# Optimization experiments

Hardware: AMD Instinct MI355X
Metric: run time of the kernel (lower is better)

## Reference

```python
import jax, jax.numpy as jnp
import numpy as np
import math

D_MODEL = 1024
NUM_HEADS = 16
HEAD_DIM = D_MODEL // NUM_HEADS  # 64
THETA = 10000.0
BATCH = 2
SEQ = 2048


def setup_inputs() -> dict:
    key = jax.random.key(0)
    ks = jax.random.split(key, 5)
    scale = 0.02
    return {
        "in_features": jax.random.normal(ks[0], (BATCH, SEQ, D_MODEL), jnp.float32),
        "q_proj": jax.random.normal(ks[1], (D_MODEL, D_MODEL), jnp.float32) * scale,
        "k_proj": jax.random.normal(ks[2], (D_MODEL, D_MODEL), jnp.float32) * scale,
        "v_proj": jax.random.normal(ks[3], (D_MODEL, D_MODEL), jnp.float32) * scale,
        "o_proj": jax.random.normal(ks[4], (D_MODEL, D_MODEL), jnp.float32) * scale,
        "token_positions": jnp.arange(SEQ, dtype=jnp.int32),
    }


def _rope(x, token_positions):
    # x: [b, h, s, head_dim]; interleaved even/odd rotation
    half = HEAD_DIM // 2
    inv_freq = 1.0 / (THETA ** (2.0 * jnp.arange(half, dtype=x.dtype) / HEAD_DIM))
    angle = token_positions.astype(x.dtype)[:, None] * inv_freq[None, :]  # [s, half]
    cos, sin = jnp.cos(angle), jnp.sin(angle)
    x_e, x_o = x[..., ::2], x[..., 1::2]
    r_e = x_e * cos - x_o * sin
    r_o = x_e * sin + x_o * cos
    # interleave back: [..., s, half, 2] -> [..., s, head_dim]
    return jnp.stack([r_e, r_o], axis=-1).reshape(x.shape)


def reference(in_features, q_proj, k_proj, v_proj, o_proj, token_positions):
    b, s, _ = in_features.shape
    # projections: weight layout is [d_out, d_in]
    Q = jnp.einsum('bsd,kd->bsk', in_features, q_proj)
    K = jnp.einsum('bsd,kd->bsk', in_features, k_proj)
    V = jnp.einsum('bsd,kd->bsk', in_features, v_proj)
    # split heads: [b, h, s, head_dim]
    Q = Q.reshape(b, s, NUM_HEADS, HEAD_DIM).transpose(0, 2, 1, 3)
    K = K.reshape(b, s, NUM_HEADS, HEAD_DIM).transpose(0, 2, 1, 3)
    V = V.reshape(b, s, NUM_HEADS, HEAD_DIM).transpose(0, 2, 1, 3)
    Q = _rope(Q, token_positions)
    K = _rope(K, token_positions)
    scores = jnp.einsum('bhnd,bhmd->bhnm', Q, K) / math.sqrt(HEAD_DIM)
    causal = jnp.tril(jnp.ones((s, s), dtype=bool))  # [s, s]
    scores = jnp.where(causal[None, None], scores, -jnp.inf)
    attn = jax.nn.softmax(scores, axis=-1)
    out = jnp.einsum('bhnm,bhmd->bhnd', attn, V)
    out = out.transpose(0, 2, 1, 3).reshape(b, s, D_MODEL)
    return jnp.einsum('bsv,dv->bsd', out, o_proj)
```

## Files before the change

kernel.cpp:

```cpp
#include <hip/hip_runtime.h>
#include <hip/hip_bf16.h>

#define D_MODEL 1024
#define NHEAD   16
#define HDIM    64
#define SEQQ    2048
#define NBATCH  2
#define MROWS   (NBATCH * SEQQ)

typedef unsigned short u16;
typedef __attribute__((ext_vector_type(8))) short short8;
typedef __attribute__((ext_vector_type(4))) float floatx4;

__device__ __forceinline__ u16 f2b(float f) {
    union { __hip_bfloat16 h; u16 u; } cv;
    cv.h = __float2bfloat16(f);
    return cv.u;
}
__device__ __forceinline__ float b2f(u16 u) {
    return __uint_as_float(((unsigned int)u) << 16);
}
__device__ __forceinline__ short8 load8(const u16* p) {
    return *reinterpret_cast<const short8*>(p);
}
__device__ __forceinline__ void async_cp16(const void* g, void* l) {
    __builtin_amdgcn_global_load_lds(
        (const __attribute__((address_space(1))) void*)g,
        (__attribute__((address_space(3))) void*)l, 16, 0, 0);
}

__global__ void cvt_all(const float* __restrict__ X,
                        const float* __restrict__ w0, const float* __restrict__ w1,
                        const float* __restrict__ w2, const float* __restrict__ w3,
                        u16* __restrict__ xo,
                        u16* __restrict__ o0, u16* __restrict__ o1,
                        u16* __restrict__ o2, u16* __restrict__ o3) {
    const int z = blockIdx.y;
    const int n4 = (D_MODEL * D_MODEL) / 4;
    const float* in;
    u16* out;
    if (z < 4) { in = X + (size_t)z * n4 * 4;  out = xo + (size_t)z * n4 * 4; }
    else {
        in  = (z == 4) ? w0 : (z == 5) ? w1 : (z == 6) ? w2 : w3;
        out = (z == 4) ? o0 : (z == 5) ? o1 : (z == 6) ? o2 : o3;
    }
    const int i = blockIdx.x * 256 + threadIdx.x;
    float4 v = reinterpret_cast<const float4*>(in)[i];
    ushort4 o;
    o.x = f2b(v.x); o.y = f2b(v.y); o.z = f2b(v.z); o.w = f2b(v.w);
    reinterpret_cast<ushort4*>(out)[i] = o;
}

__global__ __launch_bounds__(256) void gemm_qkv(
    const u16* __restrict__ A,
    const u16* __restrict__ B0, const u16* __restrict__ B1, const u16* __restrict__ B2,
    u16* __restrict__ C0, u16* __restrict__ C1, u16* __restrict__ C2)
{
    const int K = D_MODEL, N = D_MODEL;
    const u16* Bt = (blockIdx.z == 0) ? B0 : (blockIdx.z == 1 ? B1 : B2);
    u16*       Cp = (blockIdx.z == 0) ? C0 : (blockIdx.z == 1 ? C1 : C2);

    __shared__ __attribute__((aligned(16))) u16 As[128 * 32];
    __shared__ __attribute__((aligned(16))) u16 Bs[128 * 32];

    const int tid  = threadIdx.x;
    const int w    = tid >> 6;
    const int lane = tid & 63;
    const int l15  = lane & 15;
    const int quad = lane >> 4;
    const int wm   = w >> 1, wn = w & 1;
    const int tm   = blockIdx.x * 128, tn = blockIdx.y * 128;

    floatx4 acc[4][4];
#pragma unroll
    for (int i = 0; i < 4; i++)
#pragma unroll
        for (int j = 0; j < 4; j++) {
            floatx4 z = {0.f, 0.f, 0.f, 0.f};
            acc[i][j] = z;
        }

    const int srow = lane >> 2;
    const int scol = (lane & 3) * 8;

    for (int k0 = 0; k0 < K; k0 += 32) {
#pragma unroll
        for (int ch = w; ch < 8; ch += 4) {
            async_cp16(A  + (size_t)(tm + ch * 16 + srow) * K + k0 + scol, &As[ch * 512]);
            async_cp16(Bt + (size_t)(tn + ch * 16 + srow) * K + k0 + scol, &Bs[ch * 512]);
        }
        __syncthreads();

        short8 af[4], bfr[4];
#pragma unroll
        for (int mi = 0; mi < 4; mi++)
            af[mi] = load8(&As[(wm * 64 + mi * 16 + l15) * 32 + quad * 8]);
#pragma unroll
        for (int ni = 0; ni < 4; ni++)
            bfr[ni] = load8(&Bs[(wn * 64 + ni * 16 + l15) * 32 + quad * 8]);
#pragma unroll
        for (int mi = 0; mi < 4; mi++)
#pragma unroll
            for (int ni = 0; ni < 4; ni++)
                acc[mi][ni] = __builtin_amdgcn_mfma_f32_16x16x32_bf16(af[mi], bfr[ni], acc[mi][ni], 0, 0, 0);
        __syncthreads();
    }

#pragma unroll
    for (int mi = 0; mi < 4; mi++)
#pragma unroll
        for (int ni = 0; ni < 4; ni++)
#pragma unroll
            for (int rg = 0; rg < 4; rg++) {
                int row = tm + wm * 64 + mi * 16 + quad * 4 + rg;
                int col = tn + wn * 64 + ni * 16 + l15;
                Cp[(size_t)row * N + col] = f2b(acc[mi][ni][rg]);
            }
}

__global__ void rope_qk(const u16* __restrict__ Qraw, const u16* __restrict__ Kraw,
                        const int* __restrict__ pos, u16* __restrict__ Qt, u16* __restrict__ Kt)
{
    const int gid = blockIdx.x * 256 + threadIdx.x;
    const int j = gid & 31;
    const int s = (gid >> 5) & (SEQQ - 1);
    const int h = (gid >> 16) & (NHEAD - 1);
    const int b = gid >> 20;

    const float p   = (float)pos[s];
    const float inv = expf(-(float)j * (9.210340371976184f / 32.0f));
    float sn, cs;
    sincosf(p * inv, &sn, &cs);

    const size_t ioff = ((size_t)(b * SEQQ + s)) * D_MODEL + h * HDIM + 2 * j;
    const ushort2 qp = *reinterpret_cast<const ushort2*>(&Qraw[ioff]);
    const ushort2 kp = *reinterpret_cast<const ushort2*>(&Kraw[ioff]);
    const float qe = b2f(qp.x), qo = b2f(qp.y);
    const float ke = b2f(kp.x), ko = b2f(kp.y);

    const size_t ooff = (((size_t)(b * NHEAD + h)) * SEQQ + s) * HDIM + 2 * j;
    ushort2 qr;
    qr.x = f2b((qe * cs - qo * sn) * 0.125f);
    qr.y = f2b((qe * sn + qo * cs) * 0.125f);
    ushort2 kr;
    kr.x = f2b(ke * cs - ko * sn);
    kr.y = f2b(ke * sn + ko * cs);
    *reinterpret_cast<ushort2*>(&Qt[ooff]) = qr;
    *reinterpret_cast<ushort2*>(&Kt[ooff]) = kr;
}

__global__ __launch_bounds__(256) void vtrans(const u16* __restrict__ Vraw, u16* __restrict__ Vt)
{
    __shared__ u16 tile[64][65];
    const int s0 = blockIdx.x * 64, h = blockIdx.y, b = blockIdx.z;
    const int t = threadIdx.x;
#pragma unroll
    for (int i = 0; i < 16; i++) {
        int idx = t + i * 256;
        int sl = idx >> 6, dl = idx & 63;
        tile[sl][dl] = Vraw[((size_t)(b * SEQQ + s0 + sl)) * D_MODEL + h * HDIM + dl];
    }
    __syncthreads();
#pragma unroll
    for (int i = 0; i < 16; i++) {
        int idx = t + i * 256;
        int dl = idx >> 6, sl = idx & 63;
        Vt[(((size_t)(b * NHEAD + h)) * HDIM + dl) * SEQQ + s0 + sl] = tile[sl][dl];
    }
}

__global__ __launch_bounds__(256, 2) void attn_kernel(
    const u16* __restrict__ Qt, const u16* __restrict__ Kt, const u16* __restrict__ Vt,
    u16* __restrict__ Out)
{
    const int bid  = blockIdx.x;
    const int slot = bid >> 3;
    const int col  = ((bid & 7) << 2) | (slot >> 4);
    const int pr   = slot & 15;
    const int h = col & (NHEAD - 1), b = col >> 4;

    const int tid = threadIdx.x, w = tid >> 6, lane = tid & 63;
    const int l15 = lane & 15, quad = lane >> 4;
    const size_t bh = (size_t)(b * NHEAD + h);
    const u16* Qh = Qt + bh * SEQQ * HDIM;
    const u16* Kh = Kt + bh * SEQQ * HDIM;
    const u16* Vh = Vt + bh * HDIM * SEQQ;

    __shared__ __attribute__((aligned(16))) u16 Ks[3][64 * 64];
    __shared__ __attribute__((aligned(16))) u16 Vs[3][64 * 64];
    __shared__ __attribute__((aligned(16))) u16 Plds[4][16 * 64];

    short8 ones;
#pragma unroll
    for (int i = 0; i < 8; i++) ones[i] = (short)0x3F80;

    const int rr  = lane >> 3;
    const int swz = ((lane & 7) ^ rr) * 8;
    auto stage = [&](int buf, int tt) {
        const int k0s = tt * 64;
        async_cp16(Kh + (size_t)(k0s + w * 8 + rr) * HDIM + swz,       &Ks[buf][w * 512]);
        async_cp16(Kh + (size_t)(k0s + (w + 4) * 8 + rr) * HDIM + swz, &Ks[buf][(w + 4) * 512]);
        async_cp16(Vh + (size_t)(w * 8 + rr) * SEQQ + k0s + swz,       &Vs[buf][w * 512]);
        async_cp16(Vh + (size_t)((w + 4) * 8 + rr) * SEQQ + k0s + swz, &Vs[buf][(w + 4) * 512]);
    };

    const int sw1 = ((quad)     ^ (l15 & 7)) * 8;
    const int sw2 = ((quad + 4) ^ (l15 & 7)) * 8;

    for (int phase = 0; phase < 2; ++phase) {
        const int qsub  = phase ? pr : (31 - pr);
        const int q0w   = qsub * 64 + w * 16;
        const int tmaxp = qsub;

        if (phase) {
            asm volatile("s_waitcnt vmcnt(0) lgkmcnt(0)" ::: "memory");
            __builtin_amdgcn_s_barrier();
        }

        short8 qf[2];
#pragma unroll
        for (int kk = 0; kk < 2; kk++)
            qf[kk] = load8(&Qh[(size_t)(q0w + l15) * HDIM + kk * 32 + quad * 8]);

        floatx4 O[4];
        floatx4 l_acc = {0.f, 0.f, 0.f, 0.f};
#pragma unroll
        for (int c = 0; c < 4; c++) { floatx4 z = {0.f, 0.f, 0.f, 0.f}; O[c] = z; }

        stage(0, 0);
        if (tmaxp >= 1) stage(1, 1);

        for (int t = 0; t <= tmaxp; ++t) {
            if (t < tmaxp) asm volatile("s_waitcnt vmcnt(4)" ::: "memory");
            else           asm volatile("s_waitcnt vmcnt(0)" ::: "memory");
            __builtin_amdgcn_s_barrier();
            if (t + 2 <= tmaxp) stage((t + 2) % 3, t + 2);

            const u16* KsB = &Ks[t % 3][0];
            const u16* VsB = &Vs[t % 3][0];
            const int k0 = t * 64;

            floatx4 S[4];
#pragma unroll
            for (int c = 0; c < 4; c++) {
                const int rowb = (c * 16 + l15) * 64;
                floatx4 z = {0.f, 0.f, 0.f, 0.f};
                S[c] = __builtin_amdgcn_mfma_f32_16x16x32_bf16(qf[0], load8(&KsB[rowb + sw1]), z,    0, 0, 0);
                S[c] = __builtin_amdgcn_mfma_f32_16x16x32_bf16(qf[1], load8(&KsB[rowb + sw2]), S[c], 0, 0, 0);
            }

            if (t == tmaxp) {
#pragma unroll
                for (int r = 0; r < 4; r++) {
                    const int q = q0w + quad * 4 + r;
#pragma unroll
                    for (int c = 0; c < 4; c++)
                        if (k0 + c * 16 + l15 > q) S[c][r] = -1e30f;
                }
            }

#pragma unroll
            for (int c = 0; c < 4; c++)
#pragma unroll
                for (int r = 0; r < 4; r++)
                    S[c][r] = __expf(S[c][r]);

#pragma unroll
            for (int c = 0; c < 4; c++)
#pragma unroll
                for (int r = 0; r < 4; r++) {
                    const int row = quad * 4 + r;
                    const int chs = ((c * 2 + (l15 >> 3)) ^ (row & 7)) * 8 + (l15 & 7);
                    Plds[w][row * 64 + chs] = f2b(S[c][r]);
                }
            const short8 pf0 = load8(&Plds[w][l15 * 64 + ((quad)     ^ (l15 & 7)) * 8]);
            const short8 pf1 = load8(&Plds[w][l15 * 64 + ((quad + 4) ^ (l15 & 7)) * 8]);

            l_acc = __builtin_amdgcn_mfma_f32_16x16x32_bf16(pf0, ones, l_acc, 0, 0, 0);
            l_acc = __builtin_amdgcn_mfma_f32_16x16x32_bf16(pf1, ones, l_acc, 0, 0, 0);

#pragma unroll
            for (int c2 = 0; c2 < 4; c2++) {
                const int rowb = (c2 * 16 + l15) * 64;
                O[c2] = __builtin_amdgcn_mfma_f32_16x16x32_bf16(pf0, load8(&VsB[rowb + sw1]), O[c2], 0, 0, 0);
                O[c2] = __builtin_amdgcn_mfma_f32_16x16x32_bf16(pf1, load8(&VsB[rowb + sw2]), O[c2], 0, 0, 0);
            }
        }

        float inv_l[4];
#pragma unroll
        for (int r = 0; r < 4; r++) inv_l[r] = 1.0f / l_acc[r];

#pragma unroll
        for (int c2 = 0; c2 < 4; c2++)
#pragma unroll
            for (int r = 0; r < 4; r++) {
                const int q   = q0w + quad * 4 + r;
                const int colo = h * HDIM + c2 * 16 + l15;
                Out[(size_t)(b * SEQQ + q) * D_MODEL + colo] = f2b(O[c2][r] * inv_l[r]);
            }
    }
}

__global__ __launch_bounds__(256) void gemm_o(
    const u16* __restrict__ A, const u16* __restrict__ Bt, float* __restrict__ C)
{
    const int K = D_MODEL, N = D_MODEL;
    __shared__ __attribute__((aligned(16))) u16 As[64 * 32];
    __shared__ __attribute__((aligned(16))) u16 Bs[128 * 32];

    const int tid  = threadIdx.x;
    const int w    = tid >> 6;
    const int lane = tid & 63;
    const int l15  = lane & 15;
    const int quad = lane >> 4;
    const int wm   = w >> 1, wn = w & 1;
    const int tm   = blockIdx.x * 64, tn = blockIdx.y * 128;

    floatx4 acc[2][4];
#pragma unroll
    for (int i = 0; i < 2; i++)
#pragma unroll
        for (int j = 0; j < 4; j++) {
            floatx4 z = {0.f, 0.f, 0.f, 0.f};
            acc[i][j] = z;
        }

    const int srow = lane >> 2;
    const int scol = (lane & 3) * 8;

    for (int k0 = 0; k0 < K; k0 += 32) {
#pragma unroll
        for (int ch = w; ch < 12; ch += 4) {
            if (ch < 4) async_cp16(A  + (size_t)(tm + ch * 16 + srow) * K + k0 + scol, &As[ch * 512]);
            else        async_cp16(Bt + (size_t)(tn + (ch - 4) * 16 + srow) * K + k0 + scol, &Bs[(ch - 4) * 512]);
        }
        __syncthreads();

        short8 af[2], bfr[4];
#pragma unroll
        for (int mi = 0; mi < 2; mi++)
            af[mi] = load8(&As[(wm * 32 + mi * 16 + l15) * 32 + quad * 8]);
#pragma unroll
        for (int ni = 0; ni < 4; ni++)
            bfr[ni] = load8(&Bs[(wn * 64 + ni * 16 + l15) * 32 + quad * 8]);
#pragma unroll
        for (int mi = 0; mi < 2; mi++)
#pragma unroll
            for (int ni = 0; ni < 4; ni++)
                acc[mi][ni] = __builtin_amdgcn_mfma_f32_16x16x32_bf16(af[mi], bfr[ni], acc[mi][ni], 0, 0, 0);
        __syncthreads();
    }

#pragma unroll
    for (int mi = 0; mi < 2; mi++)
#pragma unroll
        for (int ni = 0; ni < 4; ni++)
#pragma unroll
            for (int rg = 0; rg < 4; rg++) {
                int row = tm + wm * 32 + mi * 16 + quad * 4 + rg;
                int col = tn + wn * 64 + ni * 16 + l15;
                C[(size_t)row * N + col] = acc[mi][ni][rg];
            }
}

extern "C" void kernel_launch(void* const* d_in, const int* in_sizes, int n_in,
                              void* d_out, int out_size, void* d_ws, size_t ws_size,
                              hipStream_t stream)
{
    const float* X  = (const float*)d_in[0];
    const float* Wq = (const float*)d_in[1];
    const float* Wk = (const float*)d_in[2];
    const float* Wv = (const float*)d_in[3];
    const float* Wo = (const float*)d_in[4];
    const int* tpos = (const int*)d_in[5];
    float* out = (float*)d_out;
    char* ws = (char*)d_ws;

    const size_t MB = (size_t)1 << 20;
    u16* Xb   = (u16*)(ws + 0);
    u16* WqB  = (u16*)(ws + 8 * MB);
    u16* WkB  = (u16*)(ws + 10 * MB);
    u16* WvB  = (u16*)(ws + 12 * MB);
    u16* WoB  = (u16*)(ws + 14 * MB);
    u16* Qraw = (u16*)(ws + 16 * MB);
    u16* Kraw = (u16*)(ws + 24 * MB);
    u16* Vraw = (u16*)(ws + 32 * MB);
    u16* Qt   = (u16*)(ws + 40 * MB);
    u16* Kt   = (u16*)(ws + 48 * MB);
    u16* Vt   = Xb;
    u16* AOut = Qraw;

    cvt_all<<<dim3(1024, 8), 256, 0, stream>>>(X, Wq, Wk, Wv, Wo,
                                               Xb, WqB, WkB, WvB, WoB);

    gemm_qkv<<<dim3(32, 8, 3), 256, 0, stream>>>(Xb, WqB, WkB, WvB,
                                                 Qraw, Kraw, Vraw);
    rope_qk<<<8192, 256, 0, stream>>>(Qraw, Kraw, tpos, Qt, Kt);
    vtrans<<<dim3(32, 16, 2), 256, 0, stream>>>(Vraw, Vt);
    attn_kernel<<<dim3(512, 1, 1), 256, 0, stream>>>(Qt, Kt, Vt, AOut);
    gemm_o<<<dim3(64, 8), 256, 0, stream>>>(AOut, WoB, out);
}
```

Measured before the change: 189.0 us.

## Keep softmax probabilities in registers by transposing QK MFMA and remapping V loads

Swaps the MFMA operands for QK^T so each lane holds score columns that match the A-operand layout of the PV MFMA. The probabilities are then packed to bf16 in registers, which removes the per-wave LDS round trip for P and its scattered 2-byte stores. V fragments are gathered as pairs of 4-element loads with a matching permuted K ordering. The 1/sqrt(d) scale now folds in log2(e) so the exponential can use the native exp2 instruction, which costs four LDS loads per V fragment instead of two.

```diff
diff --git a/kernel.cpp b/kernel.cpp
--- a/kernel.cpp
+++ b/kernel.cpp
@@ -10,6 +10,7 @@
 
 typedef unsigned short u16;
 typedef __attribute__((ext_vector_type(8))) short short8;
+typedef __attribute__((ext_vector_type(4))) short bf16x4;
 typedef __attribute__((ext_vector_type(4))) float floatx4;
 
 __device__ __forceinline__ u16 f2b(float f) {
@@ -22,6 +23,12 @@
 }
 __device__ __forceinline__ short8 load8(const u16* p) {
     return *reinterpret_cast<const short8*>(p);
+}
+__device__ __forceinline__ bf16x4 load4v(const u16* p) {
+    return *reinterpret_cast<const bf16x4*>(p);
+}
+__device__ __forceinline__ unsigned pack2(float lo, float hi) {
+    return ((unsigned)f2b(hi) << 16) | (unsigned)f2b(lo);
 }
 __device__ __forceinline__ void async_cp16(const void* g, void* l) {
     __builtin_amdgcn_global_load_lds(
@@ -139,9 +146,10 @@
     const float ke = b2f(kp.x), ko = b2f(kp.y);
 
     const size_t ooff = (((size_t)(b * NHEAD + h)) * SEQQ + s) * HDIM + 2 * j;
+    const float qs = 0.18033688011112042f;
     ushort2 qr;
-    qr.x = f2b((qe * cs - qo * sn) * 0.125f);
-    qr.y = f2b((qe * sn + qo * cs) * 0.125f);
+    qr.x = f2b((qe * cs - qo * sn) * qs);
+    qr.y = f2b((qe * sn + qo * cs) * qs);
     ushort2 kr;
     kr.x = f2b(ke * cs - ko * sn);
     kr.y = f2b(ke * sn + ko * cs);
@@ -188,7 +196,6 @@
 
     __shared__ __attribute__((aligned(16))) u16 Ks[3][64 * 64];
     __shared__ __attribute__((aligned(16))) u16 Vs[3][64 * 64];
-    __shared__ __attribute__((aligned(16))) u16 Plds[4][16 * 64];
 
     short8 ones;
 #pragma unroll
@@ -204,8 +211,13 @@
         async_cp16(Vh + (size_t)((w + 4) * 8 + rr) * SEQQ + k0s + swz, &Vs[buf][(w + 4) * 512]);
     };
 
-    const int sw1 = ((quad)     ^ (l15 & 7)) * 8;
-    const int sw2 = ((quad + 4) ^ (l15 & 7)) * 8;
+    const int s7  = l15 & 7;
+    const int sw1 = ((quad)     ^ s7) * 8;
+    const int sw2 = ((quad + 4) ^ s7) * 8;
+    const int vo0 = (((quad >> 1)    ) ^ s7) * 8 + (quad & 1) * 4;
+    const int vo1 = (((quad >> 1) + 2) ^ s7) * 8 + (quad & 1) * 4;
+    const int vo2 = (((quad >> 1) + 4) ^ s7) * 8 + (quad & 1) * 4;
+    const int vo3 = (((quad >> 1) + 6) ^ s7) * 8 + (quad & 1) * 4;
 
     for (int phase = 0; phase < 2; ++phase) {
         const int qsub  = phase ? pr : (31 - pr);
@@ -245,45 +257,49 @@
             for (int c = 0; c < 4; c++) {
                 const int rowb = (c * 16 + l15) * 64;
                 floatx4 z = {0.f, 0.f, 0.f, 0.f};
-                S[c] = __builtin_amdgcn_mfma_f32_16x16x32_bf16(qf[0], load8(&KsB[rowb + sw1]), z,    0, 0, 0);
-                S[c] = __builtin_amdgcn_mfma_f32_16x16x32_bf16(qf[1], load8(&KsB[rowb + sw2]), S[c], 0, 0, 0);
+                S[c] = __builtin_amdgcn_mfma_f32_16x16x32_bf16(load8(&KsB[rowb + sw1]), qf[0], z,    0, 0, 0);
+                S[c] = __builtin_amdgcn_mfma_f32_16x16x32_bf16(load8(&KsB[rowb + sw2]), qf[1], S[c], 0, 0, 0);
             }
 
             if (t == tmaxp) {
-#pragma unroll
-                for (int r = 0; r < 4; r++) {
-                    const int q = q0w + quad * 4 + r;
-#pragma unroll
-                    for (int c = 0; c < 4; c++)
-                        if (k0 + c * 16 + l15 > q) S[c][r] = -1e30f;
-                }
+                const int q = q0w + l15;
+#pragma unroll
+                for (int c = 0; c < 4; c++)
+#pragma unroll
+                    for (int r = 0; r < 4; r++)
+                        if (k0 + c * 16 + quad * 4 + r > q) S[c][r] = -1e30f;
             }
 
 #pragma unroll
             for (int c = 0; c < 4; c++)
 #pragma unroll
                 for (int r = 0; r < 4; r++)
-                    S[c][r] = __expf(S[c][r]);
-
-#pragma unroll
-            for (int c = 0; c < 4; c++)
-#pragma unroll
-                for (int r = 0; r < 4; r++) {
-                    const int row = quad * 4 + r;
-                    const int chs = ((c * 2 + (l15 >> 3)) ^ (row & 7)) * 8 + (l15 & 7);
-                    Plds[w][row * 64 + chs] = f2b(S[c][r]);
-                }
-            const short8 pf0 = load8(&Plds[w][l15 * 64 + ((quad)     ^ (l15 & 7)) * 8]);
-            const short8 pf1 = load8(&Plds[w][l15 * 64 + ((quad + 4) ^ (l15 & 7)) * 8]);
-
-            l_acc = __builtin_amdgcn_mfma_f32_16x16x32_bf16(pf0, ones, l_acc, 0, 0, 0);
-            l_acc = __builtin_amdgcn_mfma_f32_16x16x32_bf16(pf1, ones, l_acc, 0, 0, 0);
+                    S[c][r] = __builtin_amdgcn_exp2f(S[c][r]);
+
+            union { short8 v; unsigned u[4]; } pf0, pf1;
+            pf0.u[0] = pack2(S[0][0], S[0][1]);
+            pf0.u[1] = pack2(S[0][2], S[0][3]);
+            pf0.u[2] = pack2(S[1][0], S[1][1]);
+            pf0.u[3] = pack2(S[1][2], S[1][3]);
+            pf1.u[0] = pack2(S[2][0], S[2][1]);
+            pf1.u[1] = pack2(S[2][2], S[2][3]);
+            pf1.u[2] = pack2(S[3][0], S[3][1]);
+            pf1.u[3] = pack2(S[3][2], S[3][3]);
+
+            l_acc = __builtin_amdgcn_mfma_f32_16x16x32_bf16(pf0.v, ones, l_acc, 0, 0, 0);
+            l_acc = __builtin_amdgcn_mfma_f32_16x16x32_bf16(pf1.v, ones, l_acc, 0, 0, 0);
 
 #pragma unroll
             for (int c2 = 0; c2 < 4; c2++) {
                 const int rowb = (c2 * 16 + l15) * 64;
-                O[c2] = __builtin_amdgcn_mfma_f32_16x16x32_bf16(pf0, load8(&VsB[rowb + sw1]), O[c2], 0, 0, 0);
-                O[c2] = __builtin_amdgcn_mfma_f32_16x16x32_bf16(pf1, load8(&VsB[rowb + sw2]), O[c2], 0, 0, 0);
+                bf16x4 a0 = load4v(&VsB[rowb + vo0]);
+                bf16x4 a1 = load4v(&VsB[rowb + vo1]);
+                bf16x4 a2 = load4v(&VsB[rowb + vo2]);
+                bf16x4 a3 = load4v(&VsB[rowb + vo3]);
+                short8 v0 = __builtin_shufflevector(a0, a1, 0, 1, 2, 3, 4, 5, 6, 7);
+                short8 v1 = __builtin_shufflevector(a2, a3, 0, 1, 2, 3, 4, 5, 6, 7);
+                O[c2] = __builtin_amdgcn_mfma_f32_16x16x32_bf16(pf0.v, v0, O[c2], 0, 0, 0);
+                O[c2] = __builtin_amdgcn_mfma_f32_16x16x32_bf16(pf1.v, v1, O[c2], 0, 0, 0);
             }
         }
 
@@ -295,7 +311,7 @@
         for (int c2 = 0; c2 < 4; c2++)
 #pragma unroll
             for (int r = 0; r < 4; r++) {
-                const int q   = q0w + quad * 4 + r;
+                const int q    = q0w + quad * 4 + r;
                 const int colo = h * HDIM + c2 * 16 + l15;
                 Out[(size_t)(b * SEQQ + q) * D_MODEL + colo] = f2b(O[c2][r] * inv_l[r]);
             }
```

New measurement: 192.0 us. Within noise of the previous version (+1.6%).
